# Kernel tuning notes

Hardware: AMD Instinct MI355X
Metric: run time of the kernel (lower is better)

## Reference

```python
import jax, jax.numpy as jnp
import numpy as np

N, D_IN, D_HID, S = 50000, 128, 128, 25
BN_EPS = 1e-5
NORM_EPS = 1e-6


def setup_inputs() -> dict:
    key = jax.random.key(0)
    ks = jax.random.split(key, 16)

    def lin(k, fan_in, shape):
        b = 1.0 / np.sqrt(fan_in)
        return jax.random.uniform(k, shape, jnp.float32, -b, b)

    return {
        "features": jax.random.normal(ks[0], (N, D_IN), jnp.float32),
        "neigh_idx1": jax.random.randint(ks[1], (N, S), 0, N, jnp.int32),
        "neigh_idx2": jax.random.randint(ks[2], (N, S), 0, N, jnp.int32),
        # aggregator1: Linear(input_dim, input_dim)
        "agg1_W": lin(ks[3], D_IN, (D_IN, D_IN)),
        "agg1_b": lin(ks[4], D_IN, (D_IN,)),
        # fc1: Linear(2*input_dim, hidden_dim)
        "fc1_W": lin(ks[5], 2 * D_IN, (2 * D_IN, D_HID)),
        "fc1_b": lin(ks[6], 2 * D_IN, (D_HID,)),
        # aggregator2: Linear(hidden_dim, hidden_dim)
        "agg2_W": lin(ks[7], D_HID, (D_HID, D_HID)),
        "agg2_b": lin(ks[8], D_HID, (D_HID,)),
        # fc2: Linear(2*hidden_dim, hidden_dim)
        "fc2_W": lin(ks[9], 2 * D_HID, (2 * D_HID, D_HID)),
        "fc2_b": lin(ks[10], 2 * D_HID, (D_HID,)),
        # BatchNorm1d(hidden_dim)
        "bn_gamma": jnp.ones((D_HID,), jnp.float32),
        "bn_beta": jnp.zeros((D_HID,), jnp.float32),
    }


def _maxpool_agg(x, neigh_idx, W, b):
    # MaxPoolAggregator: relu(Linear(neighbor feats)) then max over sampled
    # neighbors. Transform once on all nodes, then gather -> max (same math,
    # avoids redundant per-neighbor GEMM work).
    h = jax.nn.relu(x @ W + b)              # [N, d_out]
    return jnp.max(h[neigh_idx], axis=1)    # [N, S, d_out] -> [N, d_out]


def reference(features, neigh_idx1, neigh_idx2,
              agg1_W, agg1_b, fc1_W, fc1_b,
              agg2_W, agg2_b, fc2_W, fc2_b,
              bn_gamma, bn_beta):
    # ---- layer 1 ----
    agg = _maxpool_agg(features, neigh_idx1, agg1_W, agg1_b)
    x = jnp.concatenate([features, agg], axis=1) @ fc1_W + fc1_b
    x = jax.nn.relu(x)
    # BatchNorm1d (training-mode batch statistics)
    mean = jnp.mean(x, axis=0)
    var = jnp.var(x, axis=0)
    x = (x - mean) * jax.lax.rsqrt(var + BN_EPS) * bn_gamma + bn_beta
    # dropout is identity in eval
    x = x / (jnp.linalg.norm(x, axis=1, keepdims=True) + NORM_EPS)
    # ---- layer 2 ----
    agg2 = _maxpool_agg(x, neigh_idx2, agg2_W, agg2_b)
    out = jnp.concatenate([x, agg2], axis=1) @ fc2_W + fc2_b
    return out
```

## Files before the change

### kernel.cpp

```cpp
#include <hip/hip_runtime.h>
#include <stdint.h>

typedef __attribute__((ext_vector_type(8))) short bf16x8;
typedef __attribute__((ext_vector_type(8))) unsigned short u16x8;
typedef __attribute__((ext_vector_type(4))) float f32x4;

__device__ __forceinline__ float bf2f(uint16_t h) { return __uint_as_float(((uint32_t)h) << 16); }
__device__ __forceinline__ uint16_t f2bf(float f) {
  uint32_t u = __float_as_uint(f);
  u += 0x7fffu + ((u >> 16) & 1u);
  return (uint16_t)(u >> 16);
}

#define NSHADOW 64

__global__ __launch_bounds__(256) void prep_k(
    const float* __restrict__ W1, const float* __restrict__ Wf1,
    const float* __restrict__ W2, const float* __restrict__ Wf2,
    const float* __restrict__ b1, const float* __restrict__ bf1,
    const float* __restrict__ b2, const float* __restrict__ bf2,
    const float* __restrict__ gam, const float* __restrict__ bet,
    uint16_t* __restrict__ F1, uint16_t* __restrict__ Ff1,
    uint16_t* __restrict__ F2, uint16_t* __restrict__ Ff2,
    float* __restrict__ fb, float* __restrict__ fgb,
    float* __restrict__ shadow)
{
  int t = blockIdx.x * 256 + threadIdx.x;
  for (int i = t; i < NSHADOW * 256; i += 12288) shadow[i] = 0.f;
  {
    const float* W; uint16_t* D; int KTl; int g;
    if (t < 2048)      { W = W1;  D = F1;  KTl = 4; g = t; }
    else if (t < 6144) { W = Wf1; D = Ff1; KTl = 8; g = t - 2048; }
    else if (t < 8192) { W = W2;  D = F2;  KTl = 4; g = t - 6144; }
    else               { W = Wf2; D = Ff2; KTl = 8; g = t - 8192; }
    int c = g >> 6, l = g & 63;
    int tt = c / KTl, kk = c - tt * KTl;
    int m = l & 15, q = l >> 4;
    int n  = tt * 16 + m;
    int k0 = kk * 32 + q * 8;
    bf16x8 a;
#pragma unroll
    for (int j = 0; j < 8; j++) a[j] = (short)f2bf(W[(size_t)(k0 + j) * 128 + n]);
    *(bf16x8*)(D + (size_t)g * 8) = a;
  }
  if (blockIdx.x == 0) {
    int i = threadIdx.x;
    for (int j = i; j < 512; j += 256) {
      const float* src = (j < 128) ? b1 : (j < 256) ? bf1 : (j < 384) ? b2 : bf2;
      fb[j] = src[j & 127];
    }
    fgb[i] = (i < 128) ? gam[i] : bet[i & 127];
  }
}

template<int MODE>
__global__ __launch_bounds__(256) void gemm_l(
    const void* __restrict__ Av, const uint16_t* __restrict__ Wf,
    const float* __restrict__ bias, const float* __restrict__ scsh,
    uint16_t* __restrict__ D, uint16_t* __restrict__ XOUT, int M)
{
  const int lane = threadIdx.x & 63;
  const int wv   = threadIdx.x >> 6;
  const int row0 = blockIdx.x * 16;
  if (row0 >= M) return;
  const int m = lane & 15, quad = lane >> 4;
  const int arow = row0 + m;

  bf16x8 afr[4];
  if (MODE == 1) {
    const float* A = (const float*)Av;
#pragma unroll
    for (int kk = 0; kk < 4; kk++) {
      const float* p = A + (size_t)arow * 128 + kk * 32 + quad * 8;
      f32x4 f0 = *(const f32x4*)p;
      f32x4 f1 = *(const f32x4*)(p + 4);
      bf16x8 a;
      a[0] = (short)f2bf(f0[0]); a[1] = (short)f2bf(f0[1]);
      a[2] = (short)f2bf(f0[2]); a[3] = (short)f2bf(f0[3]);
      a[4] = (short)f2bf(f1[0]); a[5] = (short)f2bf(f1[1]);
      a[6] = (short)f2bf(f1[2]); a[7] = (short)f2bf(f1[3]);
      afr[kk] = a;
    }
  } else {
    const uint16_t* A = (const uint16_t*)Av;
    float xv[32];
    float ss = 0.f;
#pragma unroll
    for (int kk = 0; kk < 4; kk++) {
      const int k0 = kk * 32 + quad * 8;
      bf16x8 y8 = *(const bf16x8*)(A + (size_t)arow * 128 + k0);
      f32x4 sc0 = *(const f32x4*)(scsh + k0);
      f32x4 sc1 = *(const f32x4*)(scsh + k0 + 4);
      f32x4 sh0 = *(const f32x4*)(scsh + 128 + k0);
      f32x4 sh1 = *(const f32x4*)(scsh + 128 + k0 + 4);
#pragma unroll
      for (int j = 0; j < 4; j++) {
        float a = bf2f((uint16_t)y8[j])     * sc0[j] + sh0[j];
        float b = bf2f((uint16_t)y8[4 + j]) * sc1[j] + sh1[j];
        xv[kk * 8 + j] = a; xv[kk * 8 + 4 + j] = b;
        ss += a * a + b * b;
      }
    }
    ss += __shfl_xor(ss, 16); ss += __shfl_xor(ss, 32);
    float inv = 1.0f / (sqrtf(ss) + 1e-6f);
#pragma unroll
    for (int kk = 0; kk < 4; kk++) {
      bf16x8 a;
#pragma unroll
      for (int j = 0; j < 8; j++) a[j] = (short)f2bf(xv[kk * 8 + j] * inv);
      afr[kk] = a;
    }
  }
  if (wv == 0) {
#pragma unroll
    for (int kk = 0; kk < 4; kk++)
      *(bf16x8*)(XOUT + (size_t)arow * 128 + kk * 32 + quad * 8) = afr[kk];
  }

#pragma unroll
  for (int t2 = 0; t2 < 2; t2++) {
    const int tt = wv * 2 + t2;
    bf16x8 bfr[4];
#pragma unroll
    for (int kk = 0; kk < 4; kk++)
      bfr[kk] = *(const bf16x8*)(Wf + ((size_t)(tt * 4 + kk) * 64 + lane) * 8);
    f32x4 acc = {0.f, 0.f, 0.f, 0.f};
#pragma unroll
    for (int kk = 0; kk < 4; kk++)
      acc = __builtin_amdgcn_mfma_f32_16x16x32_bf16(afr[kk], bfr[kk], acc, 0, 0, 0);
    const int col = tt * 16 + m;
    const float bv = bias[col];
#pragma unroll
    for (int r = 0; r < 4; r++) {
      float v = fmaxf(acc[r] + bv, 0.f);
      D[(size_t)(row0 + quad * 4 + r) * 128 + col] = f2bf(v);
    }
  }
}

template<bool STATS, int ODT>
__global__ __launch_bounds__(256) void gemm_g(
    const uint16_t* __restrict__ A0, const uint16_t* __restrict__ H,
    const int* __restrict__ idx, const uint16_t* __restrict__ Wf,
    const float* __restrict__ bias, void* __restrict__ Dv,
    float* __restrict__ shadow, int M)
{
  __shared__ __align__(16) uint16_t agg[16 * 136];
  const int lane = threadIdx.x & 63;
  const int wv   = threadIdx.x >> 6;
  const int row0 = blockIdx.x * 16;
  if (row0 >= M) return;
  const int m = lane & 15, quad = lane >> 4;
  const int arow = row0 + m;

  bf16x8 afr[8];
#pragma unroll
  for (int kk = 0; kk < 4; kk++)
    afr[kk] = *(const bf16x8*)(A0 + (size_t)arow * 128 + kk * 32 + quad * 8);

  {
    const int rw = row0 + wv * 4 + quad;
    const int* ir = idx + (size_t)rw * 25;
    u16x8 mx = {0, 0, 0, 0, 0, 0, 0, 0};
#pragma unroll
    for (int b = 0; b < 3; b++) {
      const int cnt = (b == 2) ? 9 : 8;
      u16x8 v[9];
#pragma unroll
      for (int e = 0; e < 9; e++) {
        if (e < cnt) {
          uint32_t j = (uint32_t)ir[b * 8 + e];
          if (j >= (uint32_t)M) j = 0;
          v[e] = *(const u16x8*)(H + (size_t)j * 128 + m * 8);
        }
      }
#pragma unroll
      for (int e = 0; e < 9; e++) {
        if (e < cnt) {
#pragma unroll
          for (int x = 0; x < 8; x++) mx[x] = (v[e][x] > mx[x]) ? v[e][x] : mx[x];
        }
      }
    }
    *(u16x8*)(&agg[(wv * 4 + quad) * 136 + m * 8]) = mx;
  }
  __syncthreads();

#pragma unroll
  for (int kk = 0; kk < 4; kk++)
    afr[4 + kk] = *(const bf16x8*)(&agg[m * 136 + kk * 32 + quad * 8]);

#pragma unroll
  for (int t2 = 0; t2 < 2; t2++) {
    const int tt = wv * 2 + t2;
    bf16x8 bfr[8];
#pragma unroll
    for (int kk = 0; kk < 8; kk++)
      bfr[kk] = *(const bf16x8*)(Wf + ((size_t)(tt * 8 + kk) * 64 + lane) * 8);
    f32x4 acc = {0.f, 0.f, 0.f, 0.f};
#pragma unroll
    for (int kk = 0; kk < 8; kk++)
      acc = __builtin_amdgcn_mfma_f32_16x16x32_bf16(afr[kk], bfr[kk], acc, 0, 0, 0);

    const int col = tt * 16 + m;
    const float bv = bias[col];
    float vals[4];
#pragma unroll
    for (int r = 0; r < 4; r++) {
      float v = acc[r] + bv;
      if (STATS) v = fmaxf(v, 0.f);
      vals[r] = v;
      size_t oidx = (size_t)(row0 + quad * 4 + r) * 128 + col;
      if (ODT == 0) ((uint16_t*)Dv)[oidx] = f2bf(v);
      else          ((float*)Dv)[oidx] = v;
    }
    if (STATS) {
      float s = vals[0] + vals[1] + vals[2] + vals[3];
      float q = vals[0]*vals[0] + vals[1]*vals[1] + vals[2]*vals[2] + vals[3]*vals[3];
      s += __shfl_xor(s, 16); s += __shfl_xor(s, 32);
      q += __shfl_xor(q, 16); q += __shfl_xor(q, 32);
      if (quad == 0) {
        float* slot = shadow + (size_t)(blockIdx.x & (NSHADOW - 1)) * 256;
        atomicAdd(&slot[col], s);
        atomicAdd(&slot[128 + col], q);
      }
    }
  }
}

__global__ __launch_bounds__(256) void bn_fin_k(
    const float* __restrict__ shadow, const float* __restrict__ fgb,
    float* __restrict__ scsh, int M)
{
  __shared__ float ps[256], pq[256];
  const int tid = threadIdx.x;
  const int col = tid & 127, part = tid >> 7;
  float s = 0.f, q = 0.f;
#pragma unroll 8
  for (int sl = part * 32; sl < part * 32 + 32; sl++) {
    s += shadow[sl * 256 + col];
    q += shadow[sl * 256 + 128 + col];
  }
  ps[tid] = s; pq[tid] = q;
  __syncthreads();
  if (tid < 128) {
    s = ps[tid] + ps[tid + 128];
    q = pq[tid] + pq[tid + 128];
    float invN = 1.0f / (float)M;
    float mean = s * invN;
    float var  = fmaxf(q * invN - mean * mean, 0.f);
    float g = fgb[tid] * rsqrtf(var + 1e-5f);
    scsh[tid] = g;
    scsh[128 + tid] = fgb[128 + tid] - mean * g;
  }
}

extern "C" void kernel_launch(void* const* d_in, const int* in_sizes, int n_in,
                              void* d_out, int out_size, void* d_ws, size_t ws_size,
                              hipStream_t stream)
{
  const float* features = (const float*)d_in[0];
  const int*   idx1     = (const int*)d_in[1];
  const int*   idx2     = (const int*)d_in[2];
  const float* agg1_W   = (const float*)d_in[3];
  const float* agg1_b   = (const float*)d_in[4];
  const float* fc1_W    = (const float*)d_in[5];
  const float* fc1_b    = (const float*)d_in[6];
  const float* agg2_W   = (const float*)d_in[7];
  const float* agg2_b   = (const float*)d_in[8];
  const float* fc2_W    = (const float*)d_in[9];
  const float* fc2_b    = (const float*)d_in[10];
  const float* bn_g     = (const float*)d_in[11];
  const float* bn_b     = (const float*)d_in[12];

  const int N = in_sizes[0] / 128;

  char* w = (char*)d_ws;
  float* shadow = (float*)w; w += NSHADOW * 256 * 4;
  uint16_t* F1  = (uint16_t*)w; w += 128 * 128 * 2;
  uint16_t* Ff1 = (uint16_t*)w; w += 128 * 256 * 2;
  uint16_t* F2  = (uint16_t*)w; w += 128 * 128 * 2;
  uint16_t* Ff2 = (uint16_t*)w; w += 128 * 256 * 2;
  float* fb   = (float*)w; w += 512 * 4;
  float* fgb  = (float*)w; w += 256 * 4;
  float* scsh = (float*)w; w += 256 * 4;
  size_t NB = (size_t)N * 128 * 2;
  uint16_t* Xb = (uint16_t*)w; w += NB;
  uint16_t* h1 = (uint16_t*)w; w += NB;
  uint16_t* yb = (uint16_t*)w; w += NB;
  uint16_t* xb = (uint16_t*)w; w += NB;
  uint16_t* h2 = (uint16_t*)w; w += NB;

  const int tb = (N + 15) / 16;

  prep_k<<<48, 256, 0, stream>>>(agg1_W, fc1_W, agg2_W, fc2_W,
      agg1_b, fc1_b, agg2_b, fc2_b, bn_g, bn_b,
      F1, Ff1, F2, Ff2, fb, fgb, shadow);
  gemm_l<1><<<tb, 256, 0, stream>>>(features, F1, fb + 0, nullptr, h1, Xb, N);
  gemm_g<true, 0><<<tb, 256, 0, stream>>>(Xb, h1, idx1, Ff1, fb + 128, yb, shadow, N);
  bn_fin_k<<<1, 256, 0, stream>>>(shadow, fgb, scsh, N);
  gemm_l<2><<<tb, 256, 0, stream>>>(yb, F2, fb + 256, scsh, h2, xb, N);
  gemm_g<false, 1><<<tb, 256, 0, stream>>>(xb, h2, idx2, Ff2, fb + 384, d_out, nullptr, N);

  (void)n_in; (void)out_size; (void)ws_size;
}
```

Baseline: 224.0 us.

## Give each wave its own rows in gemm_l and issue all gather loads upfront

```diff
diff --git a/kernel.cpp b/kernel.cpp
--- a/kernel.cpp
+++ b/kernel.cpp
@@ -4,6 +4,7 @@
 typedef __attribute__((ext_vector_type(8))) short bf16x8;
 typedef __attribute__((ext_vector_type(8))) unsigned short u16x8;
 typedef __attribute__((ext_vector_type(4))) float f32x4;
+typedef int int4a __attribute__((ext_vector_type(4), aligned(4)));
 
 __device__ __forceinline__ float bf2f(uint16_t h) { return __uint_as_float(((uint32_t)h) << 16); }
 __device__ __forceinline__ uint16_t f2bf(float f) {
@@ -61,7 +62,7 @@
 {
   const int lane = threadIdx.x & 63;
   const int wv   = threadIdx.x >> 6;
-  const int row0 = blockIdx.x * 16;
+  const int row0 = blockIdx.x * 64 + wv * 16;
   if (row0 >= M) return;
   const int m = lane & 15, quad = lane >> 4;
   const int arow = row0 + m;
@@ -111,15 +112,12 @@
       afr[kk] = a;
     }
   }
-  if (wv == 0) {
-#pragma unroll
-    for (int kk = 0; kk < 4; kk++)
-      *(bf16x8*)(XOUT + (size_t)arow * 128 + kk * 32 + quad * 8) = afr[kk];
-  }
-
-#pragma unroll
-  for (int t2 = 0; t2 < 2; t2++) {
-    const int tt = wv * 2 + t2;
+#pragma unroll
+  for (int kk = 0; kk < 4; kk++)
+    *(bf16x8*)(XOUT + (size_t)arow * 128 + kk * 32 + quad * 8) = afr[kk];
+
+#pragma unroll
+  for (int tt = 0; tt < 8; tt++) {
     bf16x8 bfr[4];
 #pragma unroll
     for (int kk = 0; kk < 4; kk++)
@@ -139,7 +137,7 @@
 }
 
 template<bool STATS, int ODT>
-__global__ __launch_bounds__(256) void gemm_g(
+__global__ __launch_bounds__(256, 3) void gemm_g(
     const uint16_t* __restrict__ A0, const uint16_t* __restrict__ H,
     const int* __restrict__ idx, const uint16_t* __restrict__ Wf,
     const float* __restrict__ bias, void* __restrict__ Dv,
@@ -161,26 +159,27 @@
   {
     const int rw = row0 + wv * 4 + quad;
     const int* ir = idx + (size_t)rw * 25;
-    u16x8 mx = {0, 0, 0, 0, 0, 0, 0, 0};
-#pragma unroll
-    for (int b = 0; b < 3; b++) {
-      const int cnt = (b == 2) ? 9 : 8;
-      u16x8 v[9];
-#pragma unroll
-      for (int e = 0; e < 9; e++) {
-        if (e < cnt) {
-          uint32_t j = (uint32_t)ir[b * 8 + e];
-          if (j >= (uint32_t)M) j = 0;
-          v[e] = *(const u16x8*)(H + (size_t)j * 128 + m * 8);
-        }
-      }
-#pragma unroll
-      for (int e = 0; e < 9; e++) {
-        if (e < cnt) {
-#pragma unroll
-          for (int x = 0; x < 8; x++) mx[x] = (v[e][x] > mx[x]) ? v[e][x] : mx[x];
-        }
-      }
+    int ii[25];
+#pragma unroll
+    for (int b = 0; b < 6; b++) {
+      int4a t4 = *(const int4a*)(ir + b * 4);
+      ii[b * 4 + 0] = t4[0]; ii[b * 4 + 1] = t4[1];
+      ii[b * 4 + 2] = t4[2]; ii[b * 4 + 3] = t4[3];
+    }
+    ii[24] = ir[24];
+    u16x8 v[25];
+#pragma unroll
+    for (int e = 0; e < 25; e++) {
+      uint32_t j = (uint32_t)ii[e];
+      if (j >= (uint32_t)M) j = 0;
+      v[e] = *(const u16x8*)(H + (size_t)j * 128 + m * 8);
+    }
+    __builtin_amdgcn_sched_barrier(0);
+    u16x8 mx = v[0];
+#pragma unroll
+    for (int e = 1; e < 25; e++) {
+#pragma unroll
+      for (int x = 0; x < 8; x++) mx[x] = (v[e][x] > mx[x]) ? v[e][x] : mx[x];
     }
     *(u16x8*)(&agg[(wv * 4 + quad) * 136 + m * 8]) = mx;
   }
@@ -291,15 +290,16 @@
   uint16_t* xb = (uint16_t*)w; w += NB;
   uint16_t* h2 = (uint16_t*)w; w += NB;
 
-  const int tb = (N + 15) / 16;
+  const int tb  = (N + 15) / 16;
+  const int tbl = (N + 63) / 64;
 
   prep_k<<<48, 256, 0, stream>>>(agg1_W, fc1_W, agg2_W, fc2_W,
       agg1_b, fc1_b, agg2_b, fc2_b, bn_g, bn_b,
       F1, Ff1, F2, Ff2, fb, fgb, shadow);
-  gemm_l<1><<<tb, 256, 0, stream>>>(features, F1, fb + 0, nullptr, h1, Xb, N);
+  gemm_l<1><<<tbl, 256, 0, stream>>>(features, F1, fb + 0, nullptr, h1, Xb, N);
   gemm_g<true, 0><<<tb, 256, 0, stream>>>(Xb, h1, idx1, Ff1, fb + 128, yb, shadow, N);
   bn_fin_k<<<1, 256, 0, stream>>>(shadow, fgb, scsh, N);
-  gemm_l<2><<<tb, 256, 0, stream>>>(yb, F2, fb + 256, scsh, h2, xb, N);
+  gemm_l<2><<<tbl, 256, 0, stream>>>(yb, F2, fb + 256, scsh, h2, xb, N);
   gemm_g<false, 1><<<tb, 256, 0, stream>>>(xb, h2, idx2, Ff2, fb + 384, d_out, nullptr, N);
 
   (void)n_in; (void)out_size; (void)ws_size;
```

Result: faster. 212.4 us (-5.2%).
